# Kernel tuning notes

Hardware: AMD Instinct MI355X
Metric: run time of the kernel (lower is better)

Reference implementation:

```python
import jax, jax.numpy as jnp
import numpy as np

N = 20000      # atoms
E = 320000     # edges
F = 128        # node_size (hard-pinned by split(128) / expand to 384)
RBF = 20
RC = 5.0
ITERS = 3
NM = 64        # molecules in batch


def setup_inputs() -> dict:
    key = jax.random.key(0)
    ks = iter(jax.random.split(key, 64))
    def nrm(shape, scale=0.05):
        return jax.random.normal(next(ks), shape, dtype=jnp.float32) * scale
    inp = {}
    inp["z"] = jax.random.randint(next(ks), (N,), 0, 119)
    inp["graph"] = jax.random.randint(next(ks), (E, 2), 0, N)
    inp["edges_dist"] = jax.random.uniform(next(ks), (E,), minval=0.5, maxval=RC, dtype=jnp.float32)
    sense = jax.random.normal(next(ks), (E, 3), dtype=jnp.float32)
    inp["edges_sense"] = sense / jnp.linalg.norm(sense, axis=1, keepdims=True)
    inp["graph_idx"] = jnp.sort(jax.random.randint(next(ks), (N,), 0, NM))
    # parameters (stacked over ITERS message/update blocks)
    inp["emb"] = nrm((119, F), 1.0)
    inp["mw1"] = nrm((ITERS, F, F)); inp["mb1"] = nrm((ITERS, F))
    inp["mw2"] = nrm((ITERS, 3 * F, F)); inp["mb2"] = nrm((ITERS, 3 * F))
    inp["ew"] = nrm((ITERS, 3 * F, RBF)); inp["eb"] = nrm((ITERS, 3 * F))
    inp["uw"] = nrm((ITERS, F, F)); inp["vw"] = nrm((ITERS, F, F))
    inp["aw1"] = nrm((ITERS, F, 2 * F)); inp["ab1"] = nrm((ITERS, F))
    inp["aw2"] = nrm((ITERS, 3 * F, F)); inp["ab2"] = nrm((ITERS, 3 * F))
    inp["ow1"] = nrm((F, F)); inp["ob1"] = nrm((F,))
    inp["ow2"] = nrm((1, F)); inp["ob2"] = nrm((1,))
    return inp


def reference(z, graph, edges_dist, edges_sense, graph_idx,
              emb, mw1, mb1, mw2, mb2, ew, eb,
              uw, vw, aw1, ab1, aw2, ab2, ow1, ob1, ow2, ob2):
    src = graph[:, 0]   # scatter target (index_add index)
    dst = graph[:, 1]   # gather source (neighbour)
    s = emb[z]                                  # [N, F]
    v = jnp.zeros((N, 3, F), dtype=s.dtype)     # [N, 3, F]
    # edge-level precompute (same every iteration)
    n = jnp.arange(1, RBF + 1, dtype=jnp.float32)
    d = edges_dist[:, None]
    rbf = jnp.sin(n * jnp.pi * d / RC) / d                              # [E, RBF]
    cut = 0.5 * (jnp.cos(jnp.pi * edges_dist / RC) + 1.0) * (edges_dist < RC)  # [E]
    for i in range(ITERS):
        # --- Message block ---
        a = jax.nn.silu(s @ mw1[i].T + mb1[i]) @ mw2[i].T + mb2[i]      # [N, 3F]
        dist_rep = (rbf @ ew[i].T + eb[i]) * cut[:, None]               # [E, 3F]
        res = a[dst] * dist_rep                                         # [E, 3F]
        rv, rs, rd = res[:, :F], res[:, F:2 * F], res[:, 2 * F:]
        resv = v[dst] * rv[:, None, :] + edges_sense[:, :, None] * rd[:, None, :]  # [E,3,F]
        s = s + 2.0 * jax.ops.segment_sum(rs, src, num_segments=N)
        v = v + 2.0 * jax.ops.segment_sum(resv, src, num_segments=N)
        # --- Update block ---
        Uv = v @ uw[i].T                                                # [N,3,F]
        Vv = v @ vw[i].T
        h = jnp.concatenate([s, jnp.linalg.norm(Vv, axis=1)], axis=-1)  # [N, 2F]
        a2 = jax.nn.silu(h @ aw1[i].T + ab1[i]) @ aw2[i].T + ab2[i]     # [N, 3F]
        avv, asv, ass = a2[:, :F], a2[:, F:2 * F], a2[:, 2 * F:]
        s = s + ass + asv * jnp.sum(Uv * Vv, axis=1)
        v = v + avv[:, None, :] * Uv
    out = jax.nn.silu(s @ ow1.T + ob1) @ ow2.T + ob2                    # [N, 1]
    return jax.ops.segment_sum(out, graph_idx, num_segments=NM)         # [NM, 1]
```

## Files before the change

kernel.cpp:

```cpp
#include <hip/hip_runtime.h>
#include <math.h>

#define NN 20000
#define NE 320000
#define FD 128
#define RBFN 20
#define RC_ 5.0f
#define NITER 3
#define NMOL 64
#define F3 384
#define F2 256
#define PI_ 3.14159265358979323846f
#define KB 128
#define LPAD 8
#define SDS 392

typedef __attribute__((ext_vector_type(8))) short  bf16x8;
typedef __attribute__((ext_vector_type(4))) float  floatx4;
typedef unsigned short u16;
typedef unsigned int   u32;

__device__ __forceinline__ u16 f2b(float x) {
    union { float f; unsigned int u; } v; v.f = x;
    unsigned int u = v.u;
    return (u16)((u + 0x7fffu + ((u >> 16) & 1u)) >> 16);
}
__device__ __forceinline__ float b2f(u16 x) {
    union { unsigned int u; float f; } v; v.u = ((unsigned int)x) << 16;
    return v.f;
}
__device__ __forceinline__ float blo(u32 w) {
    union { unsigned int u; float f; } v; v.u = w << 16; return v.f;
}
__device__ __forceinline__ float bhi(u32 w) {
    union { unsigned int u; float f; } v; v.u = w & 0xffff0000u; return v.f;
}
__device__ __forceinline__ u32 pack2(float a, float b) {
    return (u32)f2b(a) | ((u32)f2b(b) << 16);
}

__global__ __launch_bounds__(256) void cvt_w_kernel(
    const float* s0, int n0, const float* s1, int n1, const float* s2, int n2,
    const float* s3, int n3, const float* s4, int n4, const float* s5, int n5,
    const float* s6, int n6, u16* __restrict__ dst)
{
    int idx = blockIdx.x * 256 + threadIdx.x;
    if (idx < n0) { dst[idx] = f2b(s0[idx]); return; } idx -= n0; dst += n0;
    if (idx < n1) { dst[idx] = f2b(s1[idx]); return; } idx -= n1; dst += n1;
    if (idx < n2) { dst[idx] = f2b(s2[idx]); return; } idx -= n2; dst += n2;
    if (idx < n3) { dst[idx] = f2b(s3[idx]); return; } idx -= n3; dst += n3;
    if (idx < n4) { dst[idx] = f2b(s4[idx]); return; } idx -= n4; dst += n4;
    if (idx < n5) { dst[idx] = f2b(s5[idx]); return; } idx -= n5; dst += n5;
    if (idx < n6) { dst[idx] = f2b(s6[idx]); }
}

__global__ __launch_bounds__(256) void cvt_ew_kernel(const float* __restrict__ ew,
    u16* __restrict__ ewb)
{
    int idx = blockIdx.x * 256 + threadIdx.x;
    if (idx >= NITER * F3 * 32) return;
    int k = idx & 31;
    int row = idx >> 5;
    ewb[idx] = (k < RBFN) ? f2b(ew[row * RBFN + k]) : (u16)0;
}

__global__ __launch_bounds__(256) void init_kernel(const int* __restrict__ z,
    const float* __restrict__ emb, float* __restrict__ s, u16* __restrict__ sbf,
    float* __restrict__ v_a, int* __restrict__ v_pk_i)
{
    int idx = blockIdx.x * 256 + threadIdx.x;
    if (idx < NN * F3) v_a[idx] = 0.f;
    if (idx < NN * F3 / 2) v_pk_i[idx] = 0;
    if (idx < NN * FD) {
        int n = idx >> 7, f = idx & 127;
        float v = emb[z[n] * FD + f];
        s[idx] = v; sbf[idx] = f2b(v);
    }
}

__global__ __launch_bounds__(256) void zero_i_kernel(int* __restrict__ p, int n)
{
    int idx = blockIdx.x * 256 + threadIdx.x;
    if (idx < n) p[idx] = 0;
}

__global__ __launch_bounds__(256) void csr_count_kernel(const int* __restrict__ graph,
    int* __restrict__ cnt)
{
    int e = blockIdx.x * 256 + threadIdx.x;
    if (e >= NE) return;
    atomicAdd(&cnt[graph[2 * e]], 1);
}

__global__ __launch_bounds__(1024) void csr_scan_kernel(const int* __restrict__ cnt,
    int* __restrict__ row_ptr, int* __restrict__ cursor)
{
    __shared__ int sd[1024];
    int tid = threadIdx.x;
    const int chunk = (NN + 1023) / 1024;
    int start = tid * chunk;
    int end = start + chunk; if (end > NN) end = NN;
    int sum = 0;
    for (int j = start; j < end; j++) sum += cnt[j];
    sd[tid] = sum;
    __syncthreads();
    for (int off = 1; off < 1024; off <<= 1) {
        int v = 0;
        if (tid >= off) v = sd[tid - off];
        __syncthreads();
        if (tid >= off) sd[tid] += v;
        __syncthreads();
    }
    int run = (tid == 0) ? 0 : sd[tid - 1];
    for (int j = start; j < end; j++) {
        row_ptr[j] = run;
        cursor[j]  = run;
        run += cnt[j];
    }
    if (tid == 0) row_ptr[NN] = NE;
}

__global__ __launch_bounds__(256) void csr_scatter_kernel(const int* __restrict__ graph,
    int* __restrict__ cursor, int* __restrict__ edge_list)
{
    int e = blockIdx.x * 256 + threadIdx.x;
    if (e >= NE) return;
    int p = atomicAdd(&cursor[graph[2 * e]], 1);
    edge_list[p] = e;
}

__global__ __launch_bounds__(256) void edge_stream_kernel(
    const int* __restrict__ edge_list, const int* __restrict__ graph,
    const float* __restrict__ dist, const float* __restrict__ sense,
    u16* __restrict__ rbf_bf, float* __restrict__ cut_p,
    float* __restrict__ sense_p, int* __restrict__ dst_p)
{
    int j = blockIdx.x * 256 + threadIdx.x;
    if (j >= NE) return;
    int e = edge_list[j];
    float d = dist[e];
    float inv = 1.f / d;
    float base = PI_ * d / RC_;
    float s1, c1;
    __sincosf(base, &s1, &c1);
    float twoc = c1 + c1;
    u16* rb = rbf_bf + (size_t)j * 32;
    float sprev = 0.f, scur = s1;
    #pragma unroll
    for (int k = 0; k < RBFN; k++) {
        rb[k] = f2b(scur * inv);
        float snext = twoc * scur - sprev;
        sprev = scur; scur = snext;
    }
    #pragma unroll
    for (int k = RBFN; k < 32; k++) rb[k] = 0;
    cut_p[j] = 0.5f * (c1 + 1.f) * (d < RC_ ? 1.f : 0.f);
    dst_p[j] = graph[2 * e + 1];
    sense_p[3 * j + 0] = sense[3 * e + 0];
    sense_p[3 * j + 1] = sense[3 * e + 1];
    sense_p[3 * j + 2] = sense[3 * e + 2];
}

template<int K1, bool PACK>
__global__ __launch_bounds__(256) void mlp_kernel(const u16* __restrict__ A,
    const u16* __restrict__ W1, const float* __restrict__ b1,
    const u16* __restrict__ W2, const float* __restrict__ b2,
    u16* __restrict__ Ob, int M)
{
    __shared__ u16 As[64][KB + LPAD];
    __shared__ u16 Ws[128][KB + LPAD];
    __shared__ u16 T[64][KB + LPAD];
    const int bm = blockIdx.x * 64;
    const int tid = threadIdx.x;
    const int wave = tid >> 6, lane = tid & 63;
    const int wm  = (wave >> 1) * 32;
    const int wn1 = (wave & 1) * 64;
    const int wn  = (wave & 1) * 32;
    const int quad = lane >> 4, lr = lane & 15;
    const int r = tid >> 2, q = tid & 3;

    floatx4 acc1[2][4];
    #pragma unroll
    for (int i = 0; i < 2; i++)
        #pragma unroll
        for (int j = 0; j < 4; j++) acc1[i][j] = (floatx4)0.f;

    for (int ko = 0; ko < K1; ko += KB) {
        {
            int gm = bm + r;
            u16* dA = &As[r][q * 32];
            if (gm < M) {
                const u16* ap = A + (size_t)gm * K1 + ko + q * 32;
                #pragma unroll
                for (int x = 0; x < 32; x += 8)
                    *(bf16x8*)&dA[x] = *(const bf16x8*)(ap + x);
            } else {
                #pragma unroll
                for (int x = 0; x < 32; x += 8)
                    *(bf16x8*)&dA[x] = (bf16x8)0;
            }
            #pragma unroll
            for (int h = 0; h < 2; h++) {
                int wr = r + h * 64;
                const u16* wp = W1 + (size_t)wr * K1 + ko + q * 32;
                u16* dW = &Ws[wr][q * 32];
                #pragma unroll
                for (int x = 0; x < 32; x += 8)
                    *(bf16x8*)&dW[x] = *(const bf16x8*)(wp + x);
            }
        }
        __syncthreads();
        #pragma unroll
        for (int kk = 0; kk < KB; kk += 32) {
            bf16x8 a0 = *(const bf16x8*)&As[wm + lr     ][kk + quad * 8];
            bf16x8 a1 = *(const bf16x8*)&As[wm + 16 + lr][kk + quad * 8];
            #pragma unroll
            for (int j = 0; j < 4; j++) {
                bf16x8 b = *(const bf16x8*)&Ws[wn1 + j * 16 + lr][kk + quad * 8];
                acc1[0][j] = __builtin_amdgcn_mfma_f32_16x16x32_bf16(a0, b, acc1[0][j], 0, 0, 0);
                acc1[1][j] = __builtin_amdgcn_mfma_f32_16x16x32_bf16(a1, b, acc1[1][j], 0, 0, 0);
            }
        }
        __syncthreads();
    }
    #pragma unroll
    for (int i = 0; i < 2; i++) {
        #pragma unroll
        for (int j = 0; j < 4; j++) {
            int col = wn1 + j * 16 + lr;
            float bb = b1[col];
            #pragma unroll
            for (int rr = 0; rr < 4; rr++) {
                int row = wm + i * 16 + quad * 4 + rr;
                float v = acc1[i][j][rr] + bb;
                v = v / (1.f + __expf(-v));
                T[row][col] = f2b(v);
            }
        }
    }
    __syncthreads();

    for (int c0 = 0; c0 < F3; c0 += 64) {
        {
            const u16* wp = W2 + (size_t)(c0 + r) * KB + q * 32;
            u16* dW = &Ws[r][q * 32];
            #pragma unroll
            for (int x = 0; x < 32; x += 8)
                *(bf16x8*)&dW[x] = *(const bf16x8*)(wp + x);
        }
        __syncthreads();
        floatx4 acc2[2][2];
        #pragma unroll
        for (int i = 0; i < 2; i++)
            #pragma unroll
            for (int j = 0; j < 2; j++) acc2[i][j] = (floatx4)0.f;
        #pragma unroll
        for (int kk = 0; kk < KB; kk += 32) {
            bf16x8 a0 = *(const bf16x8*)&T[wm + lr     ][kk + quad * 8];
            bf16x8 a1 = *(const bf16x8*)&T[wm + 16 + lr][kk + quad * 8];
            bf16x8 b0 = *(const bf16x8*)&Ws[wn + lr     ][kk + quad * 8];
            bf16x8 b1 = *(const bf16x8*)&Ws[wn + 16 + lr][kk + quad * 8];
            acc2[0][0] = __builtin_amdgcn_mfma_f32_16x16x32_bf16(a0, b0, acc2[0][0], 0, 0, 0);
            acc2[0][1] = __builtin_amdgcn_mfma_f32_16x16x32_bf16(a0, b1, acc2[0][1], 0, 0, 0);
            acc2[1][0] = __builtin_amdgcn_mfma_f32_16x16x32_bf16(a1, b0, acc2[1][0], 0, 0, 0);
            acc2[1][1] = __builtin_amdgcn_mfma_f32_16x16x32_bf16(a1, b1, acc2[1][1], 0, 0, 0);
        }
        #pragma unroll
        for (int i = 0; i < 2; i++) {
            #pragma unroll
            for (int j = 0; j < 2; j++) {
                int gn = c0 + wn + j * 16 + lr;
                float bb = b2[gn];
                #pragma unroll
                for (int rr = 0; rr < 4; rr++) {
                    int gm = bm + wm + i * 16 + quad * 4 + rr;
                    if (gm < M) {
                        u16 val = f2b(acc2[i][j][rr] + bb);
                        if (PACK) {
                            int off = (gn < 256) ? ((gn & 127) * 2 + (gn >> 7))
                                                 : (256 + (gn & 127));
                            Ob[(size_t)gm * F3 + off] = val;
                        } else {
                            Ob[(size_t)gm * F3 + gn] = val;
                        }
                    }
                }
            }
        }
        __syncthreads();
    }
}

__global__ __launch_bounds__(256) void gemm_uv(const u16* __restrict__ A,
    const u16* __restrict__ Wu, const u16* __restrict__ Wv,
    u16* __restrict__ U, u16* __restrict__ V, int M)
{
    __shared__ u16 As[64][KB + LPAD];
    __shared__ u16 Bu[64][KB + LPAD];
    __shared__ u16 Bv[64][KB + LPAD];
    const int bm = blockIdx.x * 64;
    const int bn = blockIdx.y * 64;
    const int tid = threadIdx.x;
    const int r = tid >> 2;
    const int q = tid & 3;
    const int wave = tid >> 6;
    const int lane = tid & 63;
    const int wm = (wave >> 1) * 32;
    const int wn = (wave & 1) * 32;
    const int quad = lane >> 4;
    const int lr = lane & 15;

    floatx4 au[2][2], av[2][2];
    #pragma unroll
    for (int i = 0; i < 2; i++)
        #pragma unroll
        for (int j = 0; j < 2; j++) { au[i][j] = (floatx4)0.f; av[i][j] = (floatx4)0.f; }

    {
        int gm = bm + r;
        u16* dA = &As[r][q * 32];
        if (gm < M) {
            const u16* ap = A + (size_t)gm * KB + q * 32;
            #pragma unroll
            for (int x = 0; x < 32; x += 8)
                *(bf16x8*)&dA[x] = *(const bf16x8*)(ap + x);
        } else {
            #pragma unroll
            for (int x = 0; x < 32; x += 8)
                *(bf16x8*)&dA[x] = (bf16x8)0;
        }
        int gn = bn + r;
        const u16* up = Wu + (size_t)gn * KB + q * 32;
        const u16* vp = Wv + (size_t)gn * KB + q * 32;
        u16* dU = &Bu[r][q * 32];
        u16* dV = &Bv[r][q * 32];
        #pragma unroll
        for (int x = 0; x < 32; x += 8) {
            *(bf16x8*)&dU[x] = *(const bf16x8*)(up + x);
            *(bf16x8*)&dV[x] = *(const bf16x8*)(vp + x);
        }
    }
    __syncthreads();
    #pragma unroll
    for (int kk = 0; kk < KB; kk += 32) {
        bf16x8 a0 = *(const bf16x8*)&As[wm + lr     ][kk + quad * 8];
        bf16x8 a1 = *(const bf16x8*)&As[wm + 16 + lr][kk + quad * 8];
        bf16x8 u0 = *(const bf16x8*)&Bu[wn + lr     ][kk + quad * 8];
        bf16x8 u1 = *(const bf16x8*)&Bu[wn + 16 + lr][kk + quad * 8];
        bf16x8 v0 = *(const bf16x8*)&Bv[wn + lr     ][kk + quad * 8];
        bf16x8 v1 = *(const bf16x8*)&Bv[wn + 16 + lr][kk + quad * 8];
        au[0][0] = __builtin_amdgcn_mfma_f32_16x16x32_bf16(a0, u0, au[0][0], 0, 0, 0);
        au[0][1] = __builtin_amdgcn_mfma_f32_16x16x32_bf16(a0, u1, au[0][1], 0, 0, 0);
        au[1][0] = __builtin_amdgcn_mfma_f32_16x16x32_bf16(a1, u0, au[1][0], 0, 0, 0);
        au[1][1] = __builtin_amdgcn_mfma_f32_16x16x32_bf16(a1, u1, au[1][1], 0, 0, 0);
        av[0][0] = __builtin_amdgcn_mfma_f32_16x16x32_bf16(a0, v0, av[0][0], 0, 0, 0);
        av[0][1] = __builtin_amdgcn_mfma_f32_16x16x32_bf16(a0, v1, av[0][1], 0, 0, 0);
        av[1][0] = __builtin_amdgcn_mfma_f32_16x16x32_bf16(a1, v0, av[1][0], 0, 0, 0);
        av[1][1] = __builtin_amdgcn_mfma_f32_16x16x32_bf16(a1, v1, av[1][1], 0, 0, 0);
    }
    #pragma unroll
    for (int i = 0; i < 2; i++) {
        #pragma unroll
        for (int j = 0; j < 2; j++) {
            int gn = bn + wn + j * 16 + lr;
            #pragma unroll
            for (int rr = 0; rr < 4; rr++) {
                int gm = bm + wm + i * 16 + quad * 4 + rr;
                if (gm < M) {
                    U[(size_t)gm * FD + gn] = f2b(au[i][j][rr]);
                    V[(size_t)gm * FD + gn] = f2b(av[i][j][rr]);
                }
            }
        }
    }
}

__global__ __launch_bounds__(256) void edge_mfma_kernel(
    const u16* __restrict__ rbf_bf, const float* __restrict__ cut_p,
    const float* __restrict__ sense_p, const int* __restrict__ dst_p,
    const u16* __restrict__ ewb, const float* __restrict__ eb,
    const u16* __restrict__ a_pk, const float* __restrict__ s_in,
    const float* __restrict__ v_in, const u16* __restrict__ v_pk,
    const int* __restrict__ row_ptr,
    float* __restrict__ s_out, u16* __restrict__ s_obf,
    float* __restrict__ v_out, u16* __restrict__ v_obf)
{
    __shared__ u16   sdrep[16 * SDS];
    __shared__ float scut[16];
    __shared__ float ssen[16][4];
    __shared__ int   sdst[16];
    __shared__ float red[4 * 128];

    const int n = blockIdx.x;
    const int tid = threadIdx.x;
    const int wave = tid >> 6;
    const int lane = tid & 63;
    const int quad = lane >> 4;
    const int lr = lane & 15;
    const int f = tid & 127;
    const int half = tid >> 7;

    int beg = row_ptr[n], end = row_ptr[n + 1];
    float accs = 0.f, accv0 = 0.f, accv1 = 0.f, accv2 = 0.f;

    for (int t0 = beg; t0 < end; t0 += 16) {
        int cnt = end - t0; if (cnt > 16) cnt = 16;
        __syncthreads();
        if (tid < 16) {
            scut[tid] = (tid < cnt) ? cut_p[t0 + tid] : 0.f;
            sdst[tid] = (tid < cnt) ? dst_p[t0 + tid] : 0;
        }
        if (tid >= 64 && tid < 64 + 3 * cnt) {
            int x = tid - 64;
            ssen[x / 3][x % 3] = sense_p[3 * t0 + x];
        }
        bf16x8 afrag;
        int ge = t0 + lr;
        if (ge < end) afrag = *(const bf16x8*)&rbf_bf[(size_t)ge * 32 + quad * 8];
        else          afrag = (bf16x8)0;
        floatx4 dacc[6];
        #pragma unroll
        for (int nt = 0; nt < 6; nt++) {
            int nrow = (wave * 6 + nt) * 16 + lr;
            bf16x8 bfrag = *(const bf16x8*)&ewb[(size_t)nrow * 32 + quad * 8];
            dacc[nt] = __builtin_amdgcn_mfma_f32_16x16x32_bf16(afrag, bfrag, (floatx4)0.f, 0, 0, 0);
        }
        __syncthreads();
        #pragma unroll
        for (int nt = 0; nt < 6; nt++) {
            int ncol = (wave * 6 + nt) * 16 + lr;
            float ebn = eb[ncol];
            #pragma unroll
            for (int rr = 0; rr < 4; rr++) {
                int e = quad * 4 + rr;
                sdrep[e * SDS + ncol] = f2b((dacc[nt][rr] + ebn) * scut[e]);
            }
        }
        __syncthreads();
        int nh = cnt - half * 8; if (nh > 8) nh = 8;
        for (int k = 0; k < nh; k++) {
            int e = half * 8 + k;
            int dst = sdst[e];
            const u16* sr = &sdrep[e * SDS];
            float drv = b2f(sr[f]);
            float drs = b2f(sr[FD + f]);
            float drd = b2f(sr[2 * FD + f]);
            const u16* ar = a_pk + (size_t)dst * F3;
            u32 ap = *(const u32*)(ar + f * 2);
            float rv = b2f((u16)(ap & 0xffff)) * drv;
            float rs = b2f((u16)(ap >> 16))    * drs;
            float rd = b2f(ar[256 + f])        * drd;
            accs += rs;
            const u16* vr = v_pk + (size_t)dst * F3;
            u32 vp = *(const u32*)(vr + f * 2);
            accv0 += b2f((u16)(vp & 0xffff)) * rv + ssen[e][0] * rd;
            accv1 += b2f((u16)(vp >> 16))    * rv + ssen[e][1] * rd;
            accv2 += b2f(vr[256 + f])        * rv + ssen[e][2] * rd;
        }
    }
    __syncthreads();
    if (half == 1) {
        red[f] = accs; red[128 + f] = accv0; red[256 + f] = accv1; red[384 + f] = accv2;
    }
    __syncthreads();
    if (half == 0) {
        accs  += red[f];       accv0 += red[128 + f];
        accv1 += red[256 + f]; accv2 += red[384 + f];
        int nb = n * FD + f;
        float so = s_in[nb] + 2.f * accs;
        s_out[nb] = so; s_obf[nb] = f2b(so);
        int vb = n * F3 + f;
        float w0 = v_in[vb]           + 2.f * accv0;
        float w1 = v_in[vb + FD]      + 2.f * accv1;
        float w2 = v_in[vb + 2 * FD]  + 2.f * accv2;
        v_out[vb]          = w0; v_obf[vb]          = f2b(w0);
        v_out[vb + FD]     = w1; v_obf[vb + FD]     = f2b(w1);
        v_out[vb + 2 * FD] = w2; v_obf[vb + 2 * FD] = f2b(w2);
    }
}

__global__ __launch_bounds__(256) void build_h_kernel(const u16* __restrict__ sbf,
    const u16* __restrict__ Vv, u16* __restrict__ h)
{
    int idx = blockIdx.x * 256 + threadIdx.x;
    if (idx >= NN * 64) return;
    int n = idx >> 6, l = idx & 63;
    u32 sp = *(const u32*)&sbf[n * FD + 2 * l];
    int vb = n * F3 + 2 * l;
    u32 x0 = *(const u32*)&Vv[vb];
    u32 x1 = *(const u32*)&Vv[vb + FD];
    u32 x2 = *(const u32*)&Vv[vb + 2 * FD];
    *(u32*)&h[n * F2 + 2 * l] = sp;
    float a0 = blo(x0), a1 = blo(x1), a2 = blo(x2);
    float b0 = bhi(x0), b1 = bhi(x1), b2 = bhi(x2);
    float n0 = sqrtf(a0 * a0 + a1 * a1 + a2 * a2);
    float n1 = sqrtf(b0 * b0 + b1 * b1 + b2 * b2);
    *(u32*)&h[n * F2 + FD + 2 * l] = pack2(n0, n1);
}

__global__ __launch_bounds__(256) void update_kernel(const float* __restrict__ s_mid,
    const float* __restrict__ v_mid, const u16* __restrict__ a2,
    const u16* __restrict__ Uv, const u16* __restrict__ Vv,
    float* __restrict__ s_out, u16* __restrict__ s_obf,
    float* __restrict__ v_out, u16* __restrict__ v_pk)
{
    int idx = blockIdx.x * 256 + threadIdx.x;
    if (idx >= NN * 64) return;
    int n = idx >> 6, l = idx & 63;
    int vb = n * F3 + 2 * l;
    u32 u0p = *(const u32*)&Uv[vb];
    u32 u1p = *(const u32*)&Uv[vb + FD];
    u32 u2p = *(const u32*)&Uv[vb + 2 * FD];
    u32 w0p = *(const u32*)&Vv[vb];
    u32 w1p = *(const u32*)&Vv[vb + FD];
    u32 w2p = *(const u32*)&Vv[vb + 2 * FD];
    u32 avp = *(const u32*)&a2[vb];
    u32 asp = *(const u32*)&a2[vb + FD];
    u32 ssp = *(const u32*)&a2[vb + 2 * FD];
    int nb = n * FD + 2 * l;
    float2 sm  = *(const float2*)&s_mid[nb];
    float2 vm0 = *(const float2*)&v_mid[vb];
    float2 vm1 = *(const float2*)&v_mid[vb + FD];
    float2 vm2 = *(const float2*)&v_mid[vb + 2 * FD];
    float u0 = blo(u0p), u1 = blo(u1p), u2 = blo(u2p);
    float w0 = blo(w0p), w1 = blo(w1p), w2 = blo(w2p);
    float dot0 = u0 * w0 + u1 * w1 + u2 * w2;
    float avv0 = blo(avp), asv0 = blo(asp), ass0 = blo(ssp);
    float so0 = sm.x + ass0 + asv0 * dot0;
    float y00 = vm0.x + avv0 * u0;
    float y10 = vm1.x + avv0 * u1;
    float y20 = vm2.x + avv0 * u2;
    float U0 = bhi(u0p), U1 = bhi(u1p), U2 = bhi(u2p);
    float W0 = bhi(w0p), W1 = bhi(w1p), W2 = bhi(w2p);
    float dot1 = U0 * W0 + U1 * W1 + U2 * W2;
    float avv1 = bhi(avp), asv1 = bhi(asp), ass1 = bhi(ssp);
    float so1 = sm.y + ass1 + asv1 * dot1;
    float y01 = vm0.y + avv1 * U0;
    float y11 = vm1.y + avv1 * U1;
    float y21 = vm2.y + avv1 * U2;
    *(float2*)&s_out[nb] = make_float2(so0, so1);
    *(u32*)&s_obf[nb] = pack2(so0, so1);
    *(float2*)&v_out[vb]          = make_float2(y00, y01);
    *(float2*)&v_out[vb + FD]     = make_float2(y10, y11);
    *(float2*)&v_out[vb + 2 * FD] = make_float2(y20, y21);
    char* vpb = (char*)v_pk + (u32)n * (2 * F3);
    uint2 pr;
    pr.x = pack2(y00, y10);
    pr.y = pack2(y01, y11);
    *(uint2*)(vpb + 8 * l) = pr;
    *(u32*)(vpb + 512 + 4 * l) = pack2(y20, y21);
}

__global__ __launch_bounds__(256) void head_kernel(const u16* __restrict__ A,
    const u16* __restrict__ W1, const float* __restrict__ b1,
    const float* __restrict__ ow2, const float* __restrict__ ob2,
    float* __restrict__ nodeval)
{
    __shared__ u16 As[64][KB + LPAD];
    __shared__ u16 Ws[128][KB + LPAD];
    __shared__ float T[64][KB + 4];
    __shared__ float ow2s[KB];
    const int bm = blockIdx.x * 64;
    const int tid = threadIdx.x;
    const int wave = tid >> 6, lane = tid & 63;
    const int wm  = (wave >> 1) * 32;
    const int wn1 = (wave & 1) * 64;
    const int quad = lane >> 4, lr = lane & 15;
    const int r = tid >> 2, q = tid & 3;

    if (tid < KB) ow2s[tid] = ow2[tid];

    floatx4 acc1[2][4];
    #pragma unroll
    for (int i = 0; i < 2; i++)
        #pragma unroll
        for (int j = 0; j < 4; j++) acc1[i][j] = (floatx4)0.f;

    {
        int gm = bm + r;
        u16* dA = &As[r][q * 32];
        if (gm < NN) {
            const u16* ap = A + (size_t)gm * KB + q * 32;
            #pragma unroll
            for (int x = 0; x < 32; x += 8)
                *(bf16x8*)&dA[x] = *(const bf16x8*)(ap + x);
        } else {
            #pragma unroll
            for (int x = 0; x < 32; x += 8)
                *(bf16x8*)&dA[x] = (bf16x8)0;
        }
        #pragma unroll
        for (int h = 0; h < 2; h++) {
            int wr = r + h * 64;
            const u16* wp = W1 + (size_t)wr * KB + q * 32;
            u16* dW = &Ws[wr][q * 32];
            #pragma unroll
            for (int x = 0; x < 32; x += 8)
                *(bf16x8*)&dW[x] = *(const bf16x8*)(wp + x);
        }
    }
    __syncthreads();
    #pragma unroll
    for (int kk = 0; kk < KB; kk += 32) {
        bf16x8 a0 = *(const bf16x8*)&As[wm + lr     ][kk + quad * 8];
        bf16x8 a1 = *(const bf16x8*)&As[wm + 16 + lr][kk + quad * 8];
        #pragma unroll
        for (int j = 0; j < 4; j++) {
            bf16x8 b = *(const bf16x8*)&Ws[wn1 + j * 16 + lr][kk + quad * 8];
            acc1[0][j] = __builtin_amdgcn_mfma_f32_16x16x32_bf16(a0, b, acc1[0][j], 0, 0, 0);
            acc1[1][j] = __builtin_amdgcn_mfma_f32_16x16x32_bf16(a1, b, acc1[1][j], 0, 0, 0);
        }
    }
    #pragma unroll
    for (int i = 0; i < 2; i++) {
        #pragma unroll
        for (int j = 0; j < 4; j++) {
            int col = wn1 + j * 16 + lr;
            float bb = b1[col];
            #pragma unroll
            for (int rr = 0; rr < 4; rr++) {
                int row = wm + i * 16 + quad * 4 + rr;
                float v = acc1[i][j][rr] + bb;
                v = v / (1.f + __expf(-v));
                T[row][col] = v;
            }
        }
    }
    __syncthreads();
    int nl = tid >> 2, seg = tid & 3;
    float v = 0.f;
    #pragma unroll
    for (int x = 0; x < 32; x++) {
        int col = seg * 32 + x;
        v += T[nl][col] * ow2s[col];
    }
    v += __shfl_down(v, 2);
    v += __shfl_down(v, 1);
    if (seg == 0) {
        int gm = bm + nl;
        if (gm < NN) nodeval[gm] = v + ob2[0];
    }
}

__global__ __launch_bounds__(1024) void mol_reduce_kernel(const float* __restrict__ nodeval,
    const int* __restrict__ gidx, float* __restrict__ out)
{
    __shared__ float mol[NMOL];
    int tid = threadIdx.x;
    if (tid < NMOL) mol[tid] = 0.f;
    __syncthreads();
    int cur = -1; float acc = 0.f;
    for (int x = tid; x < NN; x += 1024) {
        int g = gidx[x];
        float v = nodeval[x];
        if (g != cur) {
            if (cur >= 0) atomicAdd(&mol[cur], acc);
            cur = g; acc = v;
        } else acc += v;
    }
    if (cur >= 0) atomicAdd(&mol[cur], acc);
    __syncthreads();
    if (tid < NMOL) out[tid] = mol[tid];
}

extern "C" void kernel_launch(void* const* d_in, const int* in_sizes, int n_in,
                              void* d_out, int out_size, void* d_ws, size_t ws_size,
                              hipStream_t stream)
{
    const int*   z     = (const int*)d_in[0];
    const int*   graph = (const int*)d_in[1];
    const float* dist  = (const float*)d_in[2];
    const float* sense = (const float*)d_in[3];
    const int*   gidx  = (const int*)d_in[4];
    const float* emb   = (const float*)d_in[5];
    const float* mw1   = (const float*)d_in[6];
    const float* mb1   = (const float*)d_in[7];
    const float* mw2   = (const float*)d_in[8];
    const float* mb2   = (const float*)d_in[9];
    const float* ew    = (const float*)d_in[10];
    const float* eb    = (const float*)d_in[11];
    const float* uw    = (const float*)d_in[12];
    const float* vw    = (const float*)d_in[13];
    const float* aw1   = (const float*)d_in[14];
    const float* ab1   = (const float*)d_in[15];
    const float* aw2   = (const float*)d_in[16];
    const float* ab2   = (const float*)d_in[17];
    const float* ow1   = (const float*)d_in[18];
    const float* ob1   = (const float*)d_in[19];
    const float* ow2   = (const float*)d_in[20];
    const float* ob2   = (const float*)d_in[21];
    float* out = (float*)d_out;

    float* W = (float*)d_ws;
    float* s_a    = W; W += (size_t)NN * FD;
    float* s_b    = W; W += (size_t)NN * FD;
    float* v_a    = W; W += (size_t)NN * F3;
    float* v_b    = W; W += (size_t)NN * F3;
    float* cut_p  = W; W += (size_t)NE;
    float* sns_p  = W; W += (size_t)NE * 3;
    float* nodeval= W; W += (size_t)NN;
    u16* U = (u16*)W;
    u16* sbf_a = U; U += (size_t)NN * FD;
    u16* sbf_b = U; U += (size_t)NN * FD;
    u16* vbf_b = U; U += (size_t)NN * F3;
    u16* a_pk  = U; U += (size_t)NN * F3;
    u16* v_pk  = U; U += (size_t)NN * F3;
    u16* h_bf  = U; U += (size_t)NN * F2;
    u16* a2_bf = U; U += (size_t)NN * F3;
    u16* Uv_bf = U; U += (size_t)NN * F3;
    u16* Vv_bf = U; U += (size_t)NN * F3;
    u16* rbf_bf= U; U += (size_t)NE * 32;
    u16* ewb   = U; U += (size_t)NITER * F3 * 32;
    u16* wb    = U; U += 557056;
    int* ip = (int*)U;
    int* row_ptr   = ip; ip += NN + 1;
    int* cnt       = ip; ip += NN;
    int* cursor    = ip; ip += NN;
    int* edge_list = ip; ip += NE;
    int* dst_p     = ip; ip += NE;

    u16* wb_mw1 = wb;
    u16* wb_mw2 = wb + 49152;
    u16* wb_uw  = wb + 196608;
    u16* wb_vw  = wb + 245760;
    u16* wb_aw1 = wb + 294912;
    u16* wb_aw2 = wb + 393216;
    u16* wb_ow1 = wb + 540672;
    const int WTOT = 557056;

    const int TB = 256;
    dim3 b256(TB);

    cvt_w_kernel<<<dim3((WTOT + TB - 1) / TB), b256, 0, stream>>>(
        mw1, 49152, mw2, 147456, uw, 49152, vw, 49152, aw1, 98304, aw2, 147456,
        ow1, 16384, wb);
    cvt_ew_kernel<<<dim3((NITER * F3 * 32 + TB - 1) / TB), b256, 0, stream>>>(ew, ewb);
    init_kernel<<<dim3((NN * F3 + TB - 1) / TB), b256, 0, stream>>>(
        z, emb, s_a, sbf_a, v_a, (int*)v_pk);
    zero_i_kernel<<<dim3((NN + TB - 1) / TB), b256, 0, stream>>>(cnt, NN);
    csr_count_kernel<<<dim3((NE + TB - 1) / TB), b256, 0, stream>>>(graph, cnt);
    csr_scan_kernel<<<dim3(1), dim3(1024), 0, stream>>>(cnt, row_ptr, cursor);
    csr_scatter_kernel<<<dim3((NE + TB - 1) / TB), b256, 0, stream>>>(graph, cursor, edge_list);
    edge_stream_kernel<<<dim3((NE + TB - 1) / TB), b256, 0, stream>>>(
        edge_list, graph, dist, sense, rbf_bf, cut_p, sns_p, dst_p);

    dim3 gM((NN + 63) / 64);
    dim3 gV2((3 * NN + 63) / 64, FD / 64);
    dim3 gPair((NN * 64 + TB - 1) / TB);

    for (int i = 0; i < NITER; i++) {
        mlp_kernel<128, true><<<gM, b256, 0, stream>>>(sbf_a,
            wb_mw1 + (size_t)i * FD * FD, mb1 + (size_t)i * FD,
            wb_mw2 + (size_t)i * F3 * FD, mb2 + (size_t)i * F3, a_pk, NN);
        edge_mfma_kernel<<<dim3(NN), b256, 0, stream>>>(
            rbf_bf, cut_p, sns_p, dst_p,
            ewb + (size_t)i * F3 * 32, eb + (size_t)i * F3,
            a_pk, s_a, v_a, v_pk, row_ptr, s_b, sbf_b, v_b, vbf_b);
        gemm_uv<<<gV2, b256, 0, stream>>>(vbf_b, wb_uw + (size_t)i * FD * FD,
            wb_vw + (size_t)i * FD * FD, Uv_bf, Vv_bf, 3 * NN);
        build_h_kernel<<<gPair, b256, 0, stream>>>(sbf_b, Vv_bf, h_bf);
        mlp_kernel<256, false><<<gM, b256, 0, stream>>>(h_bf,
            wb_aw1 + (size_t)i * FD * F2, ab1 + (size_t)i * FD,
            wb_aw2 + (size_t)i * F3 * FD, ab2 + (size_t)i * F3, a2_bf, NN);
        update_kernel<<<gPair, b256, 0, stream>>>(
            s_b, v_b, a2_bf, Uv_bf, Vv_bf, s_a, sbf_a, v_a, v_pk);
    }

    head_kernel<<<gM, b256, 0, stream>>>(sbf_a, wb_ow1, ob1, ow2, ob2, nodeval);
    mol_reduce_kernel<<<dim3(1), dim3(1024), 0, stream>>>(nodeval, gidx, out);
}
```

Baseline: 907.2 us.

## Fuse build_h, update MLP and update epilogue into one kernel

Replaces three kernels (build_h, the 256-input MLP, and the elementwise update) with a single kernel per iteration. The vector norms of Vv are computed directly into shared memory as the second K-half of the first GEMM, and the second GEMM's outputs are consumed in registers to apply the s/v update. This removes the h and a2 intermediate round trips and two launches. In exchange the epilogue does scalar, poorly coalesced 2-byte and 4-byte global accesses, and the second GEMM is split into six small chunks, each followed by a barrier.

```diff
diff --git a/kernel.cpp b/kernel.cpp
--- a/kernel.cpp
+++ b/kernel.cpp
@@ -479,76 +479,231 @@
     }
 }
 
-__global__ __launch_bounds__(256) void build_h_kernel(const u16* __restrict__ sbf,
-    const u16* __restrict__ Vv, u16* __restrict__ h)
-{
-    int idx = blockIdx.x * 256 + threadIdx.x;
-    if (idx >= NN * 64) return;
-    int n = idx >> 6, l = idx & 63;
-    u32 sp = *(const u32*)&sbf[n * FD + 2 * l];
-    int vb = n * F3 + 2 * l;
-    u32 x0 = *(const u32*)&Vv[vb];
-    u32 x1 = *(const u32*)&Vv[vb + FD];
-    u32 x2 = *(const u32*)&Vv[vb + 2 * FD];
-    *(u32*)&h[n * F2 + 2 * l] = sp;
-    float a0 = blo(x0), a1 = blo(x1), a2 = blo(x2);
-    float b0 = bhi(x0), b1 = bhi(x1), b2 = bhi(x2);
-    float n0 = sqrtf(a0 * a0 + a1 * a1 + a2 * a2);
-    float n1 = sqrtf(b0 * b0 + b1 * b1 + b2 * b2);
-    *(u32*)&h[n * F2 + FD + 2 * l] = pack2(n0, n1);
-}
-
-__global__ __launch_bounds__(256) void update_kernel(const float* __restrict__ s_mid,
-    const float* __restrict__ v_mid, const u16* __restrict__ a2,
+__global__ __launch_bounds__(256) void mlp2_update_kernel(
+    const u16* __restrict__ sbf_mid, const float* __restrict__ s_mid,
+    const float* __restrict__ v_mid,
     const u16* __restrict__ Uv, const u16* __restrict__ Vv,
+    const u16* __restrict__ W1, const float* __restrict__ b1,
+    const u16* __restrict__ W2, const float* __restrict__ b2,
     float* __restrict__ s_out, u16* __restrict__ s_obf,
-    float* __restrict__ v_out, u16* __restrict__ v_pk)
-{
-    int idx = blockIdx.x * 256 + threadIdx.x;
-    if (idx >= NN * 64) return;
-    int n = idx >> 6, l = idx & 63;
-    int vb = n * F3 + 2 * l;
-    u32 u0p = *(const u32*)&Uv[vb];
-    u32 u1p = *(const u32*)&Uv[vb + FD];
-    u32 u2p = *(const u32*)&Uv[vb + 2 * FD];
-    u32 w0p = *(const u32*)&Vv[vb];
-    u32 w1p = *(const u32*)&Vv[vb + FD];
-    u32 w2p = *(const u32*)&Vv[vb + 2 * FD];
-    u32 avp = *(const u32*)&a2[vb];
-    u32 asp = *(const u32*)&a2[vb + FD];
-    u32 ssp = *(const u32*)&a2[vb + 2 * FD];
-    int nb = n * FD + 2 * l;
-    float2 sm  = *(const float2*)&s_mid[nb];
-    float2 vm0 = *(const float2*)&v_mid[vb];
-    float2 vm1 = *(const float2*)&v_mid[vb + FD];
-    float2 vm2 = *(const float2*)&v_mid[vb + 2 * FD];
-    float u0 = blo(u0p), u1 = blo(u1p), u2 = blo(u2p);
-    float w0 = blo(w0p), w1 = blo(w1p), w2 = blo(w2p);
-    float dot0 = u0 * w0 + u1 * w1 + u2 * w2;
-    float avv0 = blo(avp), asv0 = blo(asp), ass0 = blo(ssp);
-    float so0 = sm.x + ass0 + asv0 * dot0;
-    float y00 = vm0.x + avv0 * u0;
-    float y10 = vm1.x + avv0 * u1;
-    float y20 = vm2.x + avv0 * u2;
-    float U0 = bhi(u0p), U1 = bhi(u1p), U2 = bhi(u2p);
-    float W0 = bhi(w0p), W1 = bhi(w1p), W2 = bhi(w2p);
-    float dot1 = U0 * W0 + U1 * W1 + U2 * W2;
-    float avv1 = bhi(avp), asv1 = bhi(asp), ass1 = bhi(ssp);
-    float so1 = sm.y + ass1 + asv1 * dot1;
-    float y01 = vm0.y + avv1 * U0;
-    float y11 = vm1.y + avv1 * U1;
-    float y21 = vm2.y + avv1 * U2;
-    *(float2*)&s_out[nb] = make_float2(so0, so1);
-    *(u32*)&s_obf[nb] = pack2(so0, so1);
-    *(float2*)&v_out[vb]          = make_float2(y00, y01);
-    *(float2*)&v_out[vb + FD]     = make_float2(y10, y11);
-    *(float2*)&v_out[vb + 2 * FD] = make_float2(y20, y21);
-    char* vpb = (char*)v_pk + (u32)n * (2 * F3);
-    uint2 pr;
-    pr.x = pack2(y00, y10);
-    pr.y = pack2(y01, y11);
-    *(uint2*)(vpb + 8 * l) = pr;
-    *(u32*)(vpb + 512 + 4 * l) = pack2(y20, y21);
+    float* __restrict__ v_out, u16* __restrict__ v_pk, int M)
+{
+    __shared__ u16 As[64][KB + LPAD];
+    __shared__ u16 Ws[128][KB + LPAD];
+    __shared__ u16 T[64][KB + LPAD];
+    const int bm = blockIdx.x * 64;
+    const int tid = threadIdx.x;
+    const int wave = tid >> 6, lane = tid & 63;
+    const int wm  = (wave >> 1) * 32;
+    const int wn1 = (wave & 1) * 64;
+    const int wn  = (wave & 1) * 32;
+    const int quad = lane >> 4, lr = lane & 15;
+    const int r = tid >> 2, q = tid & 3;
+
+    floatx4 acc1[2][4];
+    #pragma unroll
+    for (int i = 0; i < 2; i++)
+        #pragma unroll
+        for (int j = 0; j < 4; j++) acc1[i][j] = (floatx4)0.f;
+
+    {
+        int gm = bm + r;
+        u16* dA = &As[r][q * 32];
+        if (gm < M) {
+            const u16* ap = sbf_mid + (size_t)gm * FD + q * 32;
+            #pragma unroll
+            for (int x = 0; x < 32; x += 8)
+                *(bf16x8*)&dA[x] = *(const bf16x8*)(ap + x);
+        } else {
+            #pragma unroll
+            for (int x = 0; x < 32; x += 8)
+                *(bf16x8*)&dA[x] = (bf16x8)0;
+        }
+        #pragma unroll
+        for (int h = 0; h < 2; h++) {
+            int wr = r + h * 64;
+            const u16* wp = W1 + (size_t)wr * F2 + q * 32;
+            u16* dW = &Ws[wr][q * 32];
+            #pragma unroll
+            for (int x = 0; x < 32; x += 8)
+                *(bf16x8*)&dW[x] = *(const bf16x8*)(wp + x);
+        }
+    }
+    __syncthreads();
+    #pragma unroll
+    for (int kk = 0; kk < KB; kk += 32) {
+        bf16x8 a0 = *(const bf16x8*)&As[wm + lr     ][kk + quad * 8];
+        bf16x8 a1 = *(const bf16x8*)&As[wm + 16 + lr][kk + quad * 8];
+        #pragma unroll
+        for (int j = 0; j < 4; j++) {
+            bf16x8 b = *(const bf16x8*)&Ws[wn1 + j * 16 + lr][kk + quad * 8];
+            acc1[0][j] = __builtin_amdgcn_mfma_f32_16x16x32_bf16(a0, b, acc1[0][j], 0, 0, 0);
+            acc1[1][j] = __builtin_amdgcn_mfma_f32_16x16x32_bf16(a1, b, acc1[1][j], 0, 0, 0);
+        }
+    }
+    __syncthreads();
+    {
+        int gm = bm + r;
+        u16* dA = &As[r][q * 32];
+        if (gm < M) {
+            const u16* vvp = Vv + (size_t)gm * F3 + q * 32;
+            bf16x8 c0[4], c1[4], c2[4];
+            #pragma unroll
+            for (int t = 0; t < 4; t++) {
+                c0[t] = *(const bf16x8*)(vvp + t * 8);
+                c1[t] = *(const bf16x8*)(vvp + FD + t * 8);
+                c2[t] = *(const bf16x8*)(vvp + 2 * FD + t * 8);
+            }
+            #pragma unroll
+            for (int t = 0; t < 4; t++) {
+                #pragma unroll
+                for (int x = 0; x < 8; x++) {
+                    float a = b2f((u16)c0[t][x]);
+                    float b = b2f((u16)c1[t][x]);
+                    float c = b2f((u16)c2[t][x]);
+                    dA[t * 8 + x] = f2b(sqrtf(a * a + b * b + c * c));
+                }
+            }
+        } else {
+            #pragma unroll
+            for (int x = 0; x < 32; x += 8)
+                *(bf16x8*)&dA[x] = (bf16x8)0;
+        }
+        #pragma unroll
+        for (int h = 0; h < 2; h++) {
+            int wr = r + h * 64;
+            const u16* wp = W1 + (size_t)wr * F2 + KB + q * 32;
+            u16* dW = &Ws[wr][q * 32];
+            #pragma unroll
+            for (int x = 0; x < 32; x += 8)
+                *(bf16x8*)&dW[x] = *(const bf16x8*)(wp + x);
+        }
+    }
+    __syncthreads();
+    #pragma unroll
+    for (int kk = 0; kk < KB; kk += 32) {
+        bf16x8 a0 = *(const bf16x8*)&As[wm + lr     ][kk + quad * 8];
+        bf16x8 a1 = *(const bf16x8*)&As[wm + 16 + lr][kk + quad * 8];
+        #pragma unroll
+        for (int j = 0; j < 4; j++) {
+            bf16x8 b = *(const bf16x8*)&Ws[wn1 + j * 16 + lr][kk + quad * 8];
+            acc1[0][j] = __builtin_amdgcn_mfma_f32_16x16x32_bf16(a0, b, acc1[0][j], 0, 0, 0);
+            acc1[1][j] = __builtin_amdgcn_mfma_f32_16x16x32_bf16(a1, b, acc1[1][j], 0, 0, 0);
+        }
+    }
+    __syncthreads();
+    #pragma unroll
+    for (int i = 0; i < 2; i++) {
+        #pragma unroll
+        for (int j = 0; j < 4; j++) {
+            int col = wn1 + j * 16 + lr;
+            float bb = b1[col];
+            #pragma unroll
+            for (int rr = 0; rr < 4; rr++) {
+                int row = wm + i * 16 + quad * 4 + rr;
+                float v = acc1[i][j][rr] + bb;
+                v = v / (1.f + __expf(-v));
+                T[row][col] = f2b(v);
+            }
+        }
+    }
+    __syncthreads();
+
+    float avvr[2][2][4], asvr[2][2][4];
+    #pragma unroll
+    for (int part = 0; part < 2; part++) {
+        #pragma unroll
+        for (int piece = 0; piece < 3; piece++) {
+            const int c0 = piece * 128 + part * 64;
+            {
+                const u16* wp = W2 + (size_t)(c0 + r) * KB + q * 32;
+                u16* dW = &Ws[r][q * 32];
+                #pragma unroll
+                for (int x = 0; x < 32; x += 8)
+                    *(bf16x8*)&dW[x] = *(const bf16x8*)(wp + x);
+            }
+            __syncthreads();
+            floatx4 acc2[2][2];
+            #pragma unroll
+            for (int i = 0; i < 2; i++)
+                #pragma unroll
+                for (int j = 0; j < 2; j++) acc2[i][j] = (floatx4)0.f;
+            #pragma unroll
+            for (int kk = 0; kk < KB; kk += 32) {
+                bf16x8 a0 = *(const bf16x8*)&T[wm + lr     ][kk + quad * 8];
+                bf16x8 a1 = *(const bf16x8*)&T[wm + 16 + lr][kk + quad * 8];
+                bf16x8 b0 = *(const bf16x8*)&Ws[wn + lr     ][kk + quad * 8];
+                bf16x8 b1 = *(const bf16x8*)&Ws[wn + 16 + lr][kk + quad * 8];
+                acc2[0][0] = __builtin_amdgcn_mfma_f32_16x16x32_bf16(a0, b0, acc2[0][0], 0, 0, 0);
+                acc2[0][1] = __builtin_amdgcn_mfma_f32_16x16x32_bf16(a0, b1, acc2[0][1], 0, 0, 0);
+                acc2[1][0] = __builtin_amdgcn_mfma_f32_16x16x32_bf16(a1, b0, acc2[1][0], 0, 0, 0);
+                acc2[1][1] = __builtin_amdgcn_mfma_f32_16x16x32_bf16(a1, b1, acc2[1][1], 0, 0, 0);
+            }
+            if (piece == 0) {
+                #pragma unroll
+                for (int i = 0; i < 2; i++)
+                    #pragma unroll
+                    for (int j = 0; j < 2; j++) {
+                        int gn = c0 + wn + j * 16 + lr;
+                        float bb = b2[gn];
+                        #pragma unroll
+                        for (int rr = 0; rr < 4; rr++)
+                            avvr[i][j][rr] = acc2[i][j][rr] + bb;
+                    }
+            } else if (piece == 1) {
+                #pragma unroll
+                for (int i = 0; i < 2; i++)
+                    #pragma unroll
+                    for (int j = 0; j < 2; j++) {
+                        int gn = c0 + wn + j * 16 + lr;
+                        float bb = b2[gn];
+                        #pragma unroll
+                        for (int rr = 0; rr < 4; rr++)
+                            asvr[i][j][rr] = acc2[i][j][rr] + bb;
+                    }
+            } else {
+                #pragma unroll
+                for (int i = 0; i < 2; i++) {
+                    #pragma unroll
+                    for (int j = 0; j < 2; j++) {
+                        int gn = c0 + wn + j * 16 + lr;
+                        int f  = gn - 256;
+                        float bb = b2[gn];
+                        #pragma unroll
+                        for (int rr = 0; rr < 4; rr++) {
+                            int gm = bm + wm + i * 16 + quad * 4 + rr;
+                            if (gm < M) {
+                                float ass = acc2[i][j][rr] + bb;
+                                float asv = asvr[i][j][rr];
+                                float avv = avvr[i][j][rr];
+                                int vb = gm * F3 + f;
+                                float u0 = b2f(Uv[vb]);
+                                float u1 = b2f(Uv[vb + FD]);
+                                float u2 = b2f(Uv[vb + 2 * FD]);
+                                float w0 = b2f(Vv[vb]);
+                                float w1 = b2f(Vv[vb + FD]);
+                                float w2 = b2f(Vv[vb + 2 * FD]);
+                                float dot = u0 * w0 + u1 * w1 + u2 * w2;
+                                int nb = gm * FD + f;
+                                float so = s_mid[nb] + ass + asv * dot;
+                                s_out[nb] = so; s_obf[nb] = f2b(so);
+                                float y0 = v_mid[vb]          + avv * u0;
+                                float y1 = v_mid[vb + FD]     + avv * u1;
+                                float y2 = v_mid[vb + 2 * FD] + avv * u2;
+                                v_out[vb]          = y0;
+                                v_out[vb + FD]     = y1;
+                                v_out[vb + 2 * FD] = y2;
+                                char* vpb = (char*)v_pk + (size_t)gm * (2 * F3);
+                                *(u32*)(vpb + 4 * f) = pack2(y0, y1);
+                                *(u16*)(vpb + 512 + 2 * f) = f2b(y2);
+                            }
+                        }
+                    }
+                }
+            }
+            __syncthreads();
+        }
+    }
 }
 
 __global__ __launch_bounds__(256) void head_kernel(const u16* __restrict__ A,
@@ -746,7 +901,6 @@
 
     dim3 gM((NN + 63) / 64);
     dim3 gV2((3 * NN + 63) / 64, FD / 64);
-    dim3 gPair((NN * 64 + TB - 1) / TB);
 
     for (int i = 0; i < NITER; i++) {
         mlp_kernel<128, true><<<gM, b256, 0, stream>>>(sbf_a,
@@ -758,12 +912,11 @@
             a_pk, s_a, v_a, v_pk, row_ptr, s_b, sbf_b, v_b, vbf_b);
         gemm_uv<<<gV2, b256, 0, stream>>>(vbf_b, wb_uw + (size_t)i * FD * FD,
             wb_vw + (size_t)i * FD * FD, Uv_bf, Vv_bf, 3 * NN);
-        build_h_kernel<<<gPair, b256, 0, stream>>>(sbf_b, Vv_bf, h_bf);
-        mlp_kernel<256, false><<<gM, b256, 0, stream>>>(h_bf,
+        mlp2_update_kernel<<<gM, b256, 0, stream>>>(
+            sbf_b, s_b, v_b, Uv_bf, Vv_bf,
             wb_aw1 + (size_t)i * FD * F2, ab1 + (size_t)i * FD,
-            wb_aw2 + (size_t)i * F3 * FD, ab2 + (size_t)i * F3, a2_bf, NN);
-        update_kernel<<<gPair, b256, 0, stream>>>(
-            s_b, v_b, a2_bf, Uv_bf, Vv_bf, s_a, sbf_a, v_a, v_pk);
+            wb_aw2 + (size_t)i * F3 * FD, ab2 + (size_t)i * F3,
+            s_a, sbf_a, v_a, v_pk, NN);
     }
 
     head_kernel<<<gM, b256, 0, stream>>>(sbf_a, wb_ow1, ob1, ow2, ob2, nodeval);
```

Result: faster. 873.0 us (-3.8%).
